# Kernel optimization log

Hardware: AMD Instinct MI355X
Metric: run time of the kernel (lower is better)

## Reference

```python
import jax, jax.numpy as jnp
from jax import lax
import numpy as np

N_LEVELS = 200          # triangular mesh resolution -> N = 200*201/2 = 20100 points
T = 4096                # number of applied-field time steps


def _triangle_mesh(n_levels):
    xs = np.linspace(0.0, 1.0, n_levels, dtype=np.float32)
    b, a = np.meshgrid(xs, xs, indexing='ij')
    mask = b <= a  # Preisach triangle: beta <= alpha
    return np.stack([b[mask], a[mask]], axis=-1)  # [N, 2]


def setup_inputs() -> dict:
    key = jax.random.key(0)
    k_h, k_d = jax.random.split(key)
    mesh = jnp.asarray(_triangle_mesh(N_LEVELS))          # [20100, 2]
    n = mesh.shape[0]
    return {
        'h': jax.random.uniform(k_h, (T,), dtype=jnp.float32),   # normalized fields in [0,1]
        'mesh_points': mesh,
        'raw_density': jax.random.normal(k_d, (n,), dtype=jnp.float32),
        'scale': jnp.ones((1,), dtype=jnp.float32),
        'offset': jnp.zeros((1,), dtype=jnp.float32),
    }


def reference(h, mesh_points, raw_density, scale, offset):
    beta = mesh_points[:, 0]   # [N]
    alpha = mesh_points[:, 1]  # [N]
    n = raw_density.shape[0]
    density = jax.nn.softplus(raw_density)  # [N]

    # hs = concat(0, h); previous field for each step
    h_prev = jnp.concatenate([jnp.zeros((1,), h.dtype), h[:-1]])

    one = jnp.asarray(1.0, h.dtype)

    def step(state, hp):
        hi, hpv = hp
        swept_up = jnp.where(alpha <= hi, one, state)    # field increasing
        swept_down = jnp.where(beta >= hi, -one, state)  # field decreasing
        new_state = jnp.where(hi > hpv, swept_up,
                              jnp.where(hi < hpv, swept_down, state))
        return new_state, new_state

    init_state = -jnp.ones((n,), h.dtype)  # negative saturation
    _, states = lax.scan(step, init_state, (h, h_prev))  # [T, N]

    m = states @ density / n  # [T]
    return scale * m + offset  # [T]
```

## Files before the change

### kernel.cpp

```cpp
#include <hip/hip_runtime.h>
#include <math.h>


__device__ __forceinline__ float softplus_f(float x) {
    return fmaxf(x, 0.0f) + log1pf(expf(-fabsf(x)));
}

__global__ __launch_bounds__(256) void build_rows_stats(
    const float* __restrict__ h,
    const float* __restrict__ raw,
    float* __restrict__ Cg,
    float* __restrict__ statg,
    int T, int L, int nrowblocks)
{
    const int W  = L + 1;
    const int SP = (W + 1) & ~1;
    const int nc = (T + 63) >> 6;

    const int lane = threadIdx.x & 63;
    const int wid  = threadIdx.x >> 6;
    const int nwv  = blockDim.x >> 6;

    if ((int)blockIdx.x < nrowblocks) {
        const int j = blockIdx.x * nwv + wid;
        if (j >= L) return;
        float* row = Cg + (size_t)(j + 1) * SP;
        float s[4];
        float run = 0.0f;
#pragma unroll
        for (int q = 0; q < 4; ++q) {
            const int i = 4 * lane + q;
            float d = 0.0f;
            if (i <= j) {
                const int p = L * i - (i * (i - 1)) / 2 + (j - i);
                d = softplus_f(raw[p]);
            }
            run += d; s[q] = run;
        }
        float x = run;
        for (int o = 1; o < 64; o <<= 1) {
            const float tv = __shfl_up(x, o);
            if (lane >= o) x += tv;
        }
        const float excl = x - run;
#pragma unroll
        for (int q = 0; q < 4; ++q) {
            const int i = 4 * lane + q;
            if (i <= j) row[i + 1] = excl + s[q];
        }
        const float total = __shfl(x, 63);
        for (int b = j + 2 + lane; b <= L; b += 64) row[b] = total;
        if (lane == 0) row[0] = 0.0f;
        if (j == 0) {
            for (int b = lane; b <= L; b += 64) Cg[b] = 0.0f;
        }
    } else {
        const int c = ((int)blockIdx.x - nrowblocks) * nwv + wid;
        if (c >= nc) return;
        const int i = (c << 6) + lane;
        const bool inb = (i < T);
        const float hv = inb ? h[i] : 0.0f;
        const float hp = (inb && i > 0) ? h[i - 1] : 0.0f;
        float mu = (inb && hv > hp) ? hv : -1.0f;
        float md = (inb && hv < hp) ? hv : 2.0f;
        for (int o = 1; o < 64; o <<= 1) {
            mu = fmaxf(mu, __shfl_xor(mu, o));
            md = fminf(md, __shfl_xor(md, o));
        }
        if (lane == 0) { statg[c] = mu; statg[nc + c] = md; }
    }
}

__global__ __launch_bounds__(256) void build_cols(
    float* __restrict__ Cg, int L)
{
    const int W  = L + 1;
    const int SP = (W + 1) & ~1;
    const int lane = threadIdx.x & 63;
    const int b = blockIdx.x * (blockDim.x >> 6) + (threadIdx.x >> 6);
    if (b >= W) return;

    float v[4];
    float run = 0.0f;
#pragma unroll
    for (int q = 0; q < 4; ++q) {
        const int a = 1 + 4 * lane + q;
        const float d = (a <= L) ? Cg[(size_t)a * SP + b] : 0.0f;
        run += d; v[q] = run;
    }
    float x = run;
    for (int o = 1; o < 64; o <<= 1) {
        const float tv = __shfl_up(x, o);
        if (lane >= o) x += tv;
    }
    const float excl = x - run;
#pragma unroll
    for (int q = 0; q < 4; ++q) {
        const int a = 1 + 4 * lane + q;
        if (a <= L) Cg[(size_t)a * SP + b] = excl + v[q];
    }
}

__global__ __launch_bounds__(256) void hyst_main(
    const float* __restrict__ h,
    const float* __restrict__ mesh,
    const float* __restrict__ Cg,
    const float* __restrict__ statg,
    const float* __restrict__ scale,
    const float* __restrict__ offset,
    float* __restrict__ out,
    int T, int L, int n)
{
    extern __shared__ float sm[];
    const int W  = L + 1;
    const int SP = (W + 1) & ~1;
    const int nc = (T + 63) >> 6;

    float* lh = sm;
    float* us = sm + T;
    float* dsm = us + nc;

    const int tid  = threadIdx.x;
    const int lane = tid & 63;
    const int wid  = tid >> 6;
    const int nwv  = blockDim.x >> 6;

    const int tmax = min(T - 1, (int)(blockIdx.x + 1) * nwv - 1);
    const int nh4  = (tmax + 4) >> 2;
    const float4* h4 = (const float4*)h;
    float4* lh4 = (float4*)lh;
    for (int k = tid; k < nh4; k += blockDim.x) lh4[k] = h4[k];
    const int ncb = (tmax >> 6) + 1;
    for (int k = tid; k < ncb; k += blockDim.x) {
        us[k] = statg[k]; dsm[k] = statg[nc + k];
    }

    float xsr[4];
#pragma unroll
    for (int k = 0; k < 4; ++k) {
        const int jj = lane + 64 * k;
        xsr[k] = (jj < L) ? mesh[2 * jj + 1] : 2.0f;
    }
    __syncthreads();

    const int t = blockIdx.x * nwv + wid;
    if (t >= T) return;

    float u_max = -1.0f, d_min = 2.0f;
    int Acov = 0, Bcov = L;
    int nrec = 0;
    int r_up = 0, r_lo = 0, r_Ap = 0, r_Bp = 0;
    float acc = 0.0f;

    auto flushrec = [&]() {
        if (lane < nrec) {
            float contrib;
            if (r_up) {
                contrib = Cg[r_lo * SP + r_Bp] - Cg[r_Ap * SP + r_Bp];
            } else {
                contrib = -((Cg[L * SP + r_Bp] - Cg[L * SP + r_lo])
                          - (Cg[r_Ap * SP + r_Bp] - Cg[r_Ap * SP + r_lo]));
            }
            acc += contrib;
        }
        nrec = 0;
    };
    auto count_le = [&](float v) -> int {
        return __popcll(__ballot(xsr[0] <= v)) + __popcll(__ballot(xsr[1] <= v))
             + __popcll(__ballot(xsr[2] <= v)) + __popcll(__ballot(xsr[3] <= v));
    };
    auto count_lt = [&](float v) -> int {
        return __popcll(__ballot(xsr[0] < v)) + __popcll(__ballot(xsr[1] < v))
             + __popcll(__ballot(xsr[2] < v)) + __popcll(__ballot(xsr[3] < v));
    };
    auto process_chunk = [&](int c) {
        const int i = (c << 6) + lane;
        const float hv = lh[i];
        const float hp = (i > 0) ? lh[i - 1] : 0.0f;
        const bool valid = (i <= t);
        const bool isup = valid && (hv > hp);
        const bool isdn = valid && (hv < hp);
        unsigned long long mup = __ballot(isup && hv > u_max);
        unsigned long long mdn = __ballot(isdn && hv < d_min);
        unsigned long long m = mup | mdn;
        while (m) {
            const int rl = 63 - __builtin_clzll(m);
            const float v = __shfl(hv, rl);
            if ((mup >> rl) & 1ull) {
                u_max = v;
                const int lo = count_le(v);
                if (lo > Acov) {
                    if (lane == nrec) { r_up = 1; r_lo = lo; r_Ap = Acov; r_Bp = Bcov; }
                    ++nrec;
                    Acov = lo;
                    if (nrec == 64) flushrec();
                }
            } else {
                d_min = v;
                const int lo = count_lt(v);
                if (lo < Bcov) {
                    if (lane == nrec) { r_up = 0; r_lo = lo; r_Ap = Acov; r_Bp = Bcov; }
                    ++nrec;
                    Bcov = lo;
                    if (nrec == 64) flushrec();
                }
            }
            const unsigned long long below =
                (rl == 0) ? 0ull : ((1ull << rl) - 1ull);
            mup = __ballot(isup && hv > u_max) & below;
            mdn = __ballot(isdn && hv < d_min) & below;
            m = mup | mdn;
        }
    };

    const int ct = t >> 6;
    process_chunk(ct);

    for (int g = (ct - 1) >> 6; g >= 0; --g) {
        if (Acov >= L || Bcov <= 0) break;
        const int cbase = g << 6;
        const int c = cbase + lane;
        const bool act = (c < ct);
        const float vu = act ? us[c] : -1.0f;
        const float vd = act ? dsm[c] : 2.0f;
        float su = vu, sd = vd;
        for (int o = 1; o < 64; o <<= 1) {
            su = fmaxf(su, __shfl_down(su, o));
            sd = fminf(sd, __shfl_down(sd, o));
        }
        float sue = __shfl_down(su, 1);
        float sde = __shfl_down(sd, 1);
        if (lane == 63) { sue = -1.0f; sde = 2.0f; }
        const bool enter = act && ((vu > fmaxf(u_max, sue)) ||
                                   (vd < fminf(d_min, sde)));
        unsigned long long em = __ballot(enter);
        while (em) {
            const int rl = 63 - __builtin_clzll(em);
            process_chunk(cbase + rl);
            em &= ~(1ull << rl);
            if (Acov >= L || Bcov <= 0) break;
        }
    }

    flushrec();
    if (lane == 0) acc -= Cg[L * SP + Bcov] - Cg[Acov * SP + Bcov];
    for (int o = 1; o < 64; o <<= 1) acc += __shfl_xor(acc, o);
    if (lane == 0) out[t] = scale[0] * (acc / (float)n) + offset[0];
}

extern "C" void kernel_launch(void* const* d_in, const int* in_sizes, int n_in,
                              void* d_out, int out_size, void* d_ws, size_t ws_size,
                              hipStream_t stream) {
    const float* h      = (const float*)d_in[0];
    const float* mesh   = (const float*)d_in[1];
    const float* raw    = (const float*)d_in[2];
    const float* scale  = (const float*)d_in[3];
    const float* offset = (const float*)d_in[4];
    float* out = (float*)d_out;

    const int T = in_sizes[0];
    const int n = in_sizes[2];
    const int L = (int)((sqrt(8.0 * (double)n + 1.0) - 1.0) / 2.0 + 0.5);
    const int W = L + 1;
    const int SP = (W + 1) & ~1;
    const int nc = (T + 63) / 64;

    float* Cg    = (float*)d_ws;
    float* statg = Cg + (size_t)W * SP;

    const int nrowblocks  = (L + 3) / 4;
    const int nstatblocks = (nc + 3) / 4;
    hipLaunchKernelGGL(build_rows_stats, dim3(nrowblocks + nstatblocks),
                       dim3(256), 0, stream, h, raw, Cg, statg, T, L,
                       nrowblocks);

    const int ncolblocks = (W + 3) / 4;
    hipLaunchKernelGGL(build_cols, dim3(ncolblocks), dim3(256), 0, stream,
                       Cg, L);

    const int nwv = 4;
    const int grid = (T + nwv - 1) / nwv;
    const size_t shmem = (size_t)(T + 2 * nc) * sizeof(float);
    hipLaunchKernelGGL(hyst_main, dim3(grid), dim3(256), shmem, stream,
                       h, mesh, Cg, statg, scale, offset, out, T, L, n);
}
```

Before: 24.89 us.

## Fuse row, column and stats prefix-table build into one single-block LDS kernel

The separate row-scan/stats kernel and column-scan kernel are replaced by one kernel launched as a single 1024-thread block. It builds the whole 2D cumulative density table in shared memory (about 160 KB), runs the column prefix scan serially in LDS with float2 accesses, then copies the table to global memory. This removes one kernel launch and the global round trip between the row and column passes. In exchange, the build work that was spread over many blocks now runs on a single CU, including a serial 200-step column scan and about 13 rows per wave that each wait on global loads.

```diff
diff --git a/kernel.cpp b/kernel.cpp
--- a/kernel.cpp
+++ b/kernel.cpp
@@ -6,25 +6,39 @@
     return fmaxf(x, 0.0f) + log1pf(expf(-fabsf(x)));
 }
 
-__global__ __launch_bounds__(256) void build_rows_stats(
+__global__ __launch_bounds__(1024) void build_all(
     const float* __restrict__ h,
     const float* __restrict__ raw,
     float* __restrict__ Cg,
     float* __restrict__ statg,
-    int T, int L, int nrowblocks)
+    int T, int L)
 {
+    extern __shared__ float S[];
     const int W  = L + 1;
     const int SP = (W + 1) & ~1;
     const int nc = (T + 63) >> 6;
 
-    const int lane = threadIdx.x & 63;
-    const int wid  = threadIdx.x >> 6;
+    const int tid  = threadIdx.x;
+    const int lane = tid & 63;
+    const int wid  = tid >> 6;
     const int nwv  = blockDim.x >> 6;
 
-    if ((int)blockIdx.x < nrowblocks) {
-        const int j = blockIdx.x * nwv + wid;
-        if (j >= L) return;
-        float* row = Cg + (size_t)(j + 1) * SP;
+    for (int c = wid; c < nc; c += nwv) {
+        const int i = (c << 6) + lane;
+        const bool inb = (i < T);
+        const float hv = inb ? h[i] : 0.0f;
+        const float hp = (inb && i > 0) ? h[i - 1] : 0.0f;
+        float mu = (inb && hv > hp) ? hv : -1.0f;
+        float md = (inb && hv < hp) ? hv : 2.0f;
+        for (int o = 1; o < 64; o <<= 1) {
+            mu = fmaxf(mu, __shfl_xor(mu, o));
+            md = fminf(md, __shfl_xor(md, o));
+        }
+        if (lane == 0) { statg[c] = mu; statg[nc + c] = md; }
+    }
+
+    for (int j = wid; j < L; j += nwv) {
+        float* row = S + (j + 1) * SP;
         float s[4];
         float run = 0.0f;
 #pragma unroll
@@ -51,53 +65,43 @@
         const float total = __shfl(x, 63);
         for (int b = j + 2 + lane; b <= L; b += 64) row[b] = total;
         if (lane == 0) row[0] = 0.0f;
-        if (j == 0) {
-            for (int b = lane; b <= L; b += 64) Cg[b] = 0.0f;
-        }
-    } else {
-        const int c = ((int)blockIdx.x - nrowblocks) * nwv + wid;
-        if (c >= nc) return;
-        const int i = (c << 6) + lane;
-        const bool inb = (i < T);
-        const float hv = inb ? h[i] : 0.0f;
-        const float hp = (inb && i > 0) ? h[i - 1] : 0.0f;
-        float mu = (inb && hv > hp) ? hv : -1.0f;
-        float md = (inb && hv < hp) ? hv : 2.0f;
-        for (int o = 1; o < 64; o <<= 1) {
-            mu = fmaxf(mu, __shfl_xor(mu, o));
-            md = fminf(md, __shfl_xor(md, o));
-        }
-        if (lane == 0) { statg[c] = mu; statg[nc + c] = md; }
-    }
-}
-
-__global__ __launch_bounds__(256) void build_cols(
-    float* __restrict__ Cg, int L)
-{
-    const int W  = L + 1;
-    const int SP = (W + 1) & ~1;
-    const int lane = threadIdx.x & 63;
-    const int b = blockIdx.x * (blockDim.x >> 6) + (threadIdx.x >> 6);
-    if (b >= W) return;
-
-    float v[4];
-    float run = 0.0f;
-#pragma unroll
-    for (int q = 0; q < 4; ++q) {
-        const int a = 1 + 4 * lane + q;
-        const float d = (a <= L) ? Cg[(size_t)a * SP + b] : 0.0f;
-        run += d; v[q] = run;
-    }
-    float x = run;
-    for (int o = 1; o < 64; o <<= 1) {
-        const float tv = __shfl_up(x, o);
-        if (lane >= o) x += tv;
-    }
-    const float excl = x - run;
-#pragma unroll
-    for (int q = 0; q < 4; ++q) {
-        const int a = 1 + 4 * lane + q;
-        if (a <= L) Cg[(size_t)a * SP + b] = excl + v[q];
+    }
+    if (wid == 0) {
+        for (int b = lane; b <= L; b += 64) S[b] = 0.0f;
+    }
+    __syncthreads();
+
+    if (wid < 2) {
+        const int cp = (wid << 6) + lane;
+        if (cp < (SP >> 1)) {
+            float2* S2 = (float2*)S;
+            const int rs = SP >> 1;
+            float rx = 0.0f, ry = 0.0f;
+            int a = 1;
+            for (; a + 3 <= L; a += 4) {
+                float2 v0 = S2[(a    ) * rs + cp];
+                float2 v1 = S2[(a + 1) * rs + cp];
+                float2 v2 = S2[(a + 2) * rs + cp];
+                float2 v3 = S2[(a + 3) * rs + cp];
+                rx += v0.x; ry += v0.y; S2[(a    ) * rs + cp] = make_float2(rx, ry);
+                rx += v1.x; ry += v1.y; S2[(a + 1) * rs + cp] = make_float2(rx, ry);
+                rx += v2.x; ry += v2.y; S2[(a + 2) * rs + cp] = make_float2(rx, ry);
+                rx += v3.x; ry += v3.y; S2[(a + 3) * rs + cp] = make_float2(rx, ry);
+            }
+            for (; a <= L; ++a) {
+                float2 v = S2[a * rs + cp];
+                rx += v.x; ry += v.y;
+                S2[a * rs + cp] = make_float2(rx, ry);
+            }
+        }
+    }
+    __syncthreads();
+
+    {
+        float2* Cg2 = (float2*)Cg;
+        float2* S2  = (float2*)S;
+        const int tot2 = (W * SP) >> 1;
+        for (int k = tid; k < tot2; k += blockDim.x) Cg2[k] = S2[k];
     }
 }
 
@@ -268,19 +272,16 @@
     float* Cg    = (float*)d_ws;
     float* statg = Cg + (size_t)W * SP;
 
-    const int nrowblocks  = (L + 3) / 4;
-    const int nstatblocks = (nc + 3) / 4;
-    hipLaunchKernelGGL(build_rows_stats, dim3(nrowblocks + nstatblocks),
-                       dim3(256), 0, stream, h, raw, Cg, statg, T, L,
-                       nrowblocks);
-
-    const int ncolblocks = (W + 3) / 4;
-    hipLaunchKernelGGL(build_cols, dim3(ncolblocks), dim3(256), 0, stream,
-                       Cg, L);
+    const size_t shmem1 = (size_t)W * SP * sizeof(float);
+    (void)hipFuncSetAttribute(reinterpret_cast<const void*>(build_all),
+                              hipFuncAttributeMaxDynamicSharedMemorySize,
+                              (int)shmem1);
+    hipLaunchKernelGGL(build_all, dim3(1), dim3(1024), shmem1, stream,
+                       h, raw, Cg, statg, T, L);
 
     const int nwv = 4;
     const int grid = (T + nwv - 1) / nwv;
-    const size_t shmem = (size_t)(T + 2 * nc) * sizeof(float);
-    hipLaunchKernelGGL(hyst_main, dim3(grid), dim3(256), shmem, stream,
+    const size_t shmem2 = (size_t)(T + 2 * nc) * sizeof(float);
+    hipLaunchKernelGGL(hyst_main, dim3(grid), dim3(256), shmem2, stream,
                        h, mesh, Cg, statg, scale, offset, out, T, L, n);
 }
```

New measurement: 73.62 us. 2.96x slower.
